# Kernel tuning notes

Hardware: AMD Instinct MI355X
Metric: run time of the kernel (lower is better)

## Reference

```python
import jax, jax.numpy as jnp
import numpy as np

B, T, N, CIN = 8, 12, 883, 3
C, E, H = 64, 10, 8
HD = C // H
TOPK = 48  # int(5 * log2(883))
DIL = [1, 2, 1, 2, 1, 2, 1, 2]
NEG = -9.0e15
L = 8

def _l2norm(v, ax):
    return v / jnp.maximum(jnp.linalg.norm(v, axis=ax, keepdims=True), 1e-12)

def _gelu(v):
    return jax.nn.gelu(v, approximate=False)

def setup_inputs():
    key = jax.random.key(0)
    ks = list(jax.random.split(key, 48))
    it = iter(ks)
    ch0 = jax.random.normal(next(it), (B, T, N))
    ch1 = jax.random.uniform(next(it), (B, T, N))                    # time-of-day in [0,1)
    ch2 = jax.random.randint(next(it), (B, T, N), 0, 7).astype(jnp.float32)  # day-of-week
    x = jnp.stack([ch0, ch1, ch2], axis=-1)
    def row_norm(kk):
        a = jax.random.uniform(kk, (N, N))
        return a / a.sum(axis=1, keepdims=True)
    def w(kk, shape):
        fan_in = shape[-2] if len(shape) >= 2 else shape[-1]
        return (jax.random.normal(kk, shape) * (1.0 / float(np.sqrt(fan_in)))).astype(jnp.float32)
    inp = dict(
        x=x,
        support0=row_norm(next(it)),
        support1=row_norm(next(it)),
        TiD=jax.random.normal(next(it), (288, E)) * 0.1,
        DiW=jax.random.normal(next(it), (7, E)) * 0.1,
        E1=jax.random.normal(next(it), (N, E)) * 0.1,
        E2=jax.random.normal(next(it), (N, E)) * 0.1,
        E3=jax.random.normal(next(it), (N, E)) * 0.1,
        Wx=w(next(it), (T // 2 + 1, E)),
        Wd=w(next(it), (N, 4 * E, E)),
        Wxabs=w(next(it), (E, E)),
        start_w=w(next(it), (CIN, C)), start_b=jnp.zeros((C,)),
        Wq=w(next(it), (L, C, C)), bq=jnp.zeros((L, C)),
        Wk=w(next(it), (L, C, C)), bk=jnp.zeros((L, C)),
        Wv=w(next(it), (L, C, C)), bv=jnp.zeros((L, C)),
        W1=w(next(it), (L, C, 4 * C)), b1=jnp.zeros((L, 4 * C)),
        W2=w(next(it), (L, 4 * C, C)), b2=jnp.zeros((L, C)),
        filt_w=jax.random.normal(next(it), (L, 2, C, C)) * (1.0 / float(np.sqrt(2 * C))),
        filt_b=jnp.zeros((L, C)),
        gate_w=jax.random.normal(next(it), (L, 2, C, C)) * (1.0 / float(np.sqrt(2 * C))),
        gate_b=jnp.zeros((L, C)),
        skip_w=w(next(it), (L, C, 256)), skip_b=jnp.zeros((L, 256)),
        gcn_w=w(next(it), (L, 9 * C, C)), gcn_b=jnp.zeros((L, C)),
        bn_g=jnp.ones((L, C)), bn_b=jnp.zeros((L, C)),
        end1_w=w(next(it), (256, 512)), end1_b=jnp.zeros((512,)),
        end2_w=w(next(it), (512, T)), end2_b=jnp.zeros((T,)),
    )
    return inp

def _graph_gen(xs, T_D, D_W, E3, Wx, Wd, Wxabs):
    # xs: [B,T,N] raw signal channel
    xf = jnp.abs(jnp.fft.rfft(xs, axis=1))                 # [B,F=7,N]
    xf = _l2norm(_l2norm(xf, 1), 2)
    xe = jnp.einsum('btn,td->bnd', xf, Wx)                 # [B,N,E]
    e3 = jnp.broadcast_to(E3[None], (xe.shape[0], N, E))
    xcat = jnp.concatenate([xe, e3, T_D, D_W], axis=2)     # [B,N,4E]
    x1 = jax.nn.relu(jnp.einsum('bnf,nfe->bne', xcat, Wd)) # per-node weight
    mu = x1.mean(axis=(1, 2), keepdims=True)               # LayerNorm over [N,E]
    var = ((x1 - mu) ** 2).mean(axis=(1, 2), keepdims=True)
    x1k = (x1 - mu) / jnp.sqrt(var + 1e-8)
    dew = jnp.einsum('bne,ek->bnk', x1k, Wxabs)
    adp = jax.nn.relu(jnp.einsum('bnk,bmk->bnm', dew, x1)) # [B,N,N]
    _, idx = jax.lax.top_k(adp, TOPK)                      # [B,N,K] per-row topk
    bi = jnp.arange(adp.shape[0])[:, None, None]
    ri = jnp.arange(N)[None, :, None]
    mask = jnp.zeros_like(adp).at[bi, ri, idx].set(1.0)
    return jax.nn.softmax(adp * mask, axis=2)

def reference(x, support0, support1, TiD, DiW, E1, E2, E3, Wx, Wd, Wxabs,
              start_w, start_b, Wq, bq, Wk, bk, Wv, bv, W1, b1, W2, b2,
              filt_w, filt_b, gate_w, gate_b, skip_w, skip_b,
              gcn_w, gcn_b, bn_g, bn_b, end1_w, end1_b, end2_w, end2_b):
    tid = (x[:, -1, :, 1] * 288).astype(jnp.int32)         # [B,N]
    T_D = TiD[tid]                                         # [B,N,E]
    D_W = DiW[x[:, -1, :, 2].astype(jnp.int32)]
    Adap = jax.nn.softmax(jax.nn.relu(E1 @ E2.T), axis=1)
    AD = _graph_gen(x[..., 0], T_D, D_W, E3, Wx, Wd, Wxabs)
    supports = [support0, support1, Adap, AD]

    h = jnp.transpose(x, (0, 3, 2, 1))                     # [B,3,N,T]
    h = jnp.pad(h, ((0, 0), (0, 0), (0, 0), (1, 0)))       # pad to receptive_field=13
    h = jnp.einsum('io,bint->bont', start_w, h) + start_b[None, :, None, None]

    skip = None
    for l in range(L):
        res = h
        # --- causal temporal attention ---
        Xa = jnp.transpose(h, (0, 3, 2, 1))                # [B,Tc,N,C]
        Tc = Xa.shape[1]
        q = _gelu(Xa @ Wq[l] + bq[l]).reshape(-1, Tc, N, H, HD)
        k = _gelu(Xa @ Wk[l] + bk[l]).reshape(-1, Tc, N, H, HD)
        v = _gelu(Xa @ Wv[l] + bv[l]).reshape(-1, Tc, N, H, HD)
        att = jnp.einsum('btnhd,bsnhd->bnhts', q, k) / (HD ** 0.5)
        cmask = jnp.tril(jnp.ones((Tc, Tc), bool))
        att = jax.nn.softmax(jnp.where(cmask, att, NEG), axis=-1)
        o = jnp.einsum('bnhts,bsnhd->bnthd', att, v).reshape(-1, N, Tc, C)
        o = _gelu(o @ W1[l] + b1[l]) @ W2[l] + b2[l]
        h = jnp.transpose(o, (0, 3, 1, 2)) + res           # [B,C,N,Tc]
        # --- gated dilated causal conv (kernel (1,2), dilation d) ---
        d = DIL[l]
        a0, a1 = h[..., :-d], h[..., d:]
        f = jnp.tanh(jnp.einsum('io,bint->bont', filt_w[l, 0], a0)
                     + jnp.einsum('io,bint->bont', filt_w[l, 1], a1)
                     + filt_b[l][None, :, None, None])
        g = jax.nn.sigmoid(jnp.einsum('io,bint->bont', gate_w[l, 0], a0)
                           + jnp.einsum('io,bint->bont', gate_w[l, 1], a1)
                           + gate_b[l][None, :, None, None])
        h = f * g
        s = jnp.einsum('io,bint->bont', skip_w[l], h) + skip_b[l][None, :, None, None]
        skip = s if skip is None else s + skip[..., -s.shape[3]:]
        # --- diffusion graph conv, order 2 over 4 supports ---
        out = [h]
        for a in supports:
            if a.ndim == 3:
                x1 = jnp.einsum('bcvt,bwv->bcwt', h, a)
                x2 = jnp.einsum('bcvt,bwv->bcwt', x1, a)
            else:
                x1 = jnp.einsum('bcvt,vw->bcwt', h, a)
                x2 = jnp.einsum('bcvt,vw->bcwt', x1, a)
            out += [x1, x2]
        hc = jnp.concatenate(out, axis=1)                  # [B,9C,N,Tc']
        h = jnp.einsum('io,bint->bont', gcn_w[l], hc) + gcn_b[l][None, :, None, None]
        h = h + res[..., -h.shape[3]:]
        # --- BatchNorm2d (batch statistics, training-mode normalization) ---
        mu = h.mean(axis=(0, 2, 3), keepdims=True)
        var = ((h - mu) ** 2).mean(axis=(0, 2, 3), keepdims=True)
        h = bn_g[l][None, :, None, None] * (h - mu) / jnp.sqrt(var + 1e-5) \
            + bn_b[l][None, :, None, None]

    out = jax.nn.relu(skip)
    out = jax.nn.relu(jnp.einsum('io,bint->bont', end1_w, out)
                      + end1_b[None, :, None, None])
    out = jnp.einsum('io,bint->bont', end2_w, out) + end2_b[None, :, None, None]
    return out  # [B, out_steps=12, N, 1]
```

## Files before the change

### kernel.cpp

```cpp
#include <hip/hip_runtime.h>
#include <math.h>

#define DIVUP(a,b) (((a)+(b)-1)/(b))

namespace {

constexpr int B=8, T=12, N=883, CIN=3, C=64, E=10, H=8, HD=8, TOPK=48, L=8;
constexpr int SKC=256, F7=7, T13=13;
constexpr int NP=896;

typedef __attribute__((ext_vector_type(8))) short bf16x8;
typedef __attribute__((ext_vector_type(4))) float f32x4;

__device__ __forceinline__ float geluf(float x){ return 0.5f*x*(1.0f+erff(x*0.7071067811865475f)); }
__device__ __forceinline__ float sigmf(float x){ return 1.0f/(1.0f+expf(-x)); }
__device__ __forceinline__ float us2f(unsigned short u){ return __uint_as_float(((unsigned)u)<<16); }
__device__ __forceinline__ unsigned short f2us(float f){
  unsigned x=__float_as_uint(f);
  return (unsigned short)((x + 0x7fffu + ((x>>16)&1u))>>16);
}

template<int KK, int STRIDE, int KW>
__device__ __forceinline__ f32x4 tile_mm(
    const unsigned short* sAh, const unsigned short* sAl,
    const unsigned short* __restrict__ Wh, const unsigned short* __restrict__ Wl,
    int colBase, int lane, f32x4 acc){
  int lr=lane&15, lg=lane>>4;
  #pragma unroll
  for(int k0=0;k0<KK;k0+=32){
    bf16x8 ah=*(const bf16x8*)&sAh[lr*STRIDE+k0+8*lg];
    bf16x8 al=*(const bf16x8*)&sAl[lr*STRIDE+k0+8*lg];
    bf16x8 bh=*(const bf16x8*)&Wh[(size_t)(colBase+lr)*KW+k0+8*lg];
    bf16x8 bl=*(const bf16x8*)&Wl[(size_t)(colBase+lr)*KW+k0+8*lg];
    acc=__builtin_amdgcn_mfma_f32_16x16x32_bf16(ah,bh,acc,0,0,0);
    acc=__builtin_amdgcn_mfma_f32_16x16x32_bf16(ah,bl,acc,0,0,0);
    acc=__builtin_amdgcn_mfma_f32_16x16x32_bf16(al,bh,acc,0,0,0);
  }
  return acc;
}

__global__ void k_dft(const float* __restrict__ x, float* __restrict__ xf){
  int idx = blockIdx.x*256 + threadIdx.x;
  if(idx >= B*F7*N) return;
  int n = idx % N; int f = (idx/N) % F7; int b = idx/(N*F7);
  float re=0.f, im=0.f;
  for(int t=0;t<T;t++){
    float v = x[((size_t)(b*T+t)*N+n)*CIN];
    float ang = -6.283185307179586f * (float)(f*t) / 12.0f;
    re += v*cosf(ang); im += v*sinf(ang);
  }
  xf[idx] = sqrtf(re*re+im*im);
}

__global__ void k_l2f(float* __restrict__ xf){
  int idx = blockIdx.x*256 + threadIdx.x;
  if(idx >= B*N) return;
  int n = idx % N; int b = idx / N;
  float s=0.f;
  for(int f=0;f<F7;f++){ float v=xf[((size_t)b*F7+f)*N+n]; s+=v*v; }
  float inv = 1.0f/fmaxf(sqrtf(s), 1e-12f);
  for(int f=0;f<F7;f++) xf[((size_t)b*F7+f)*N+n] *= inv;
}

__global__ void k_l2n(float* __restrict__ xf){
  int bf = blockIdx.x; int tid = threadIdx.x;
  __shared__ float red[256];
  size_t base = (size_t)bf*N;
  float s=0.f;
  for(int i=tid;i<N;i+=256){ float v=xf[base+i]; s+=v*v; }
  red[tid]=s; __syncthreads();
  for(int k=128;k>0;k>>=1){ if(tid<k) red[tid]+=red[tid+k]; __syncthreads(); }
  float inv = 1.0f/fmaxf(sqrtf(red[0]), 1e-12f);
  __syncthreads();
  for(int i=tid;i<N;i+=256) xf[base+i]*=inv;
}

__global__ void k_x1(const float* __restrict__ x, const float* __restrict__ xf,
                     const float* __restrict__ E3, const float* __restrict__ TiD,
                     const float* __restrict__ DiW, const float* __restrict__ Wx,
                     const float* __restrict__ Wd, float* __restrict__ x1){
  int idx = blockIdx.x*256+threadIdx.x;
  if(idx>=B*N) return;
  int n=idx%N, b=idx/N;
  float xc[40];
  for(int d=0;d<E;d++){
    float a=0.f;
    for(int f=0;f<F7;f++) a += xf[((size_t)b*F7+f)*N+n]*Wx[f*E+d];
    xc[d]=a;
  }
  for(int d=0;d<E;d++) xc[10+d]=E3[n*E+d];
  int ti = (int)(x[((size_t)(b*T+(T-1))*N+n)*CIN+1]*288.0f);
  int dw = (int)(x[((size_t)(b*T+(T-1))*N+n)*CIN+2]);
  for(int d=0;d<E;d++) xc[20+d]=TiD[ti*E+d];
  for(int d=0;d<E;d++) xc[30+d]=DiW[dw*E+d];
  for(int e=0;e<E;e++){
    float a=0.f;
    for(int f=0;f<40;f++) a += xc[f]*Wd[((size_t)n*40+f)*E+e];
    x1[(size_t)idx*E+e]=fmaxf(a,0.f);
  }
}

__global__ void k_lnstats(const float* __restrict__ x1, float* __restrict__ st){
  int b=blockIdx.x, tid=threadIdx.x;
  __shared__ float rs[256], rq[256];
  const int M=N*E;
  float s=0.f,q=0.f;
  for(int i=tid;i<M;i+=256){ float v=x1[(size_t)b*M+i]; s+=v; q+=v*v; }
  rs[tid]=s; rq[tid]=q; __syncthreads();
  for(int k=128;k>0;k>>=1){ if(tid<k){ rs[tid]+=rs[tid+k]; rq[tid]+=rq[tid+k]; } __syncthreads(); }
  if(tid==0){ float mu=rs[0]/M; float var=rq[0]/M-mu*mu; st[b*2]=mu; st[b*2+1]=var; }
}

__global__ void k_dew(const float* __restrict__ x1, const float* __restrict__ st,
                      const float* __restrict__ Wxabs, float* __restrict__ dew){
  int idx=blockIdx.x*256+threadIdx.x;
  if(idx>=B*N) return;
  int b=idx/N;
  float mu=st[b*2], var=st[b*2+1];
  float rs=rsqrtf(var+1e-8f);
  float xk[E];
  for(int e=0;e<E;e++) xk[e]=(x1[(size_t)idx*E+e]-mu)*rs;
  for(int k=0;k<E;k++){
    float a=0.f;
    for(int e=0;e<E;e++) a+=xk[e]*Wxabs[e*E+k];
    dew[(size_t)idx*E+k]=a;
  }
}

__global__ void k_adp(const float* __restrict__ dew, const float* __restrict__ x1,
                      float* __restrict__ adp){
  size_t idx=(size_t)blockIdx.x*256+threadIdx.x;
  if(idx>=(size_t)B*N*N) return;
  int m=(int)(idx%N); int n=(int)((idx/N)%N); int b=(int)(idx/((size_t)N*N));
  const float* dr=dew+((size_t)b*N+n)*E;
  const float* xr=x1+((size_t)b*N+m)*E;
  float a=0.f;
  for(int k=0;k<E;k++) a+=dr[k]*xr[k];
  adp[idx]=fmaxf(a,0.f);
}

__global__ __launch_bounds__(256) void k_topk(const float* __restrict__ adp,
                       unsigned short* __restrict__ ADhi, unsigned short* __restrict__ ADlo){
  int row = blockIdx.x*4 + (threadIdx.x>>6);
  int lane = threadIdx.x & 63;
  const float* rp = adp + (size_t)row*N;
  float v[14];
  #pragma unroll
  for(int j=0;j<14;j++){
    int i = lane + j*64;
    v[j] = (i<N) ? rp[i] : -1.f;
  }
  unsigned sel = 0u;
  float m0 = 0.f;
  for(int k=0;k<TOPK;k++){
    float bv = -2.f; int bi = 1<<20;
    #pragma unroll
    for(int j=0;j<14;j++){
      if(!((sel>>j)&1u) && v[j] > bv){ bv = v[j]; bi = lane + j*64; }
    }
    #pragma unroll
    for(int off=1; off<64; off<<=1){
      float ov = __shfl_xor(bv, off);
      int   oi = __shfl_xor(bi, off);
      if(ov > bv || (ov==bv && oi<bi)){ bv=ov; bi=oi; }
    }
    if(k==0) m0 = bv;
    if((bi&63)==lane) sel |= 1u << (bi>>6);
  }
  float pv[14];
  float ls = 0.f;
  #pragma unroll
  for(int j=0;j<14;j++){
    int i = lane + j*64;
    float p = ((sel>>j)&1u) ? v[j] : 0.f;
    pv[j] = p;
    if(i<N) ls += expf(p - m0);
  }
  #pragma unroll
  for(int off=1; off<64; off<<=1) ls += __shfl_xor(ls, off);
  float invZ = 1.f/ls;
  size_t base = ((size_t)(row/N)*NP + (size_t)(row%N))*NP;
  #pragma unroll
  for(int j=0;j<14;j++){
    int i = lane + j*64;
    if(i<N){
      float f = expf(pv[j]-m0)*invZ;
      unsigned short h=f2us(f);
      ADhi[base+i]=h; ADlo[base+i]=f2us(f-us2f(h));
    }
  }
}

__global__ void k_adap(const float* __restrict__ E1, const float* __restrict__ E2,
                       unsigned short* __restrict__ Mh, unsigned short* __restrict__ Ml){
  int v=blockIdx.x, tid=threadIdx.x;
  __shared__ float rowv[N];
  __shared__ float rv[256];
  float e1[E];
  for(int e=0;e<E;e++) e1[e]=E1[v*E+e];
  for(int j=tid;j<N;j+=256){
    float s=0.f;
    for(int e=0;e<E;e++) s+=e1[e]*E2[j*E+e];
    rowv[j]=fmaxf(s,0.f);
  }
  __syncthreads();
  float lm=-1e30f;
  for(int j=tid;j<N;j+=256) lm=fmaxf(lm,rowv[j]);
  rv[tid]=lm; __syncthreads();
  for(int s=128;s>0;s>>=1){ if(tid<s) rv[tid]=fmaxf(rv[tid],rv[tid+s]); __syncthreads(); }
  float m=rv[0]; __syncthreads();
  float ls=0.f;
  for(int j=tid;j<N;j+=256) ls+=expf(rowv[j]-m);
  rv[tid]=ls; __syncthreads();
  for(int s=128;s>0;s>>=1){ if(tid<s) rv[tid]+=rv[tid+s]; __syncthreads(); }
  float invZ=1.0f/rv[0];
  for(int j=tid;j<N;j+=256){
    float f=expf(rowv[j]-m)*invZ;
    unsigned short h=f2us(f);
    Mh[(size_t)j*NP+v]=h; Ml[(size_t)j*NP+v]=f2us(f-us2f(h));
  }
}

__global__ void k_cvtT(const float* __restrict__ A, unsigned short* __restrict__ Mh,
                       unsigned short* __restrict__ Ml){
  int idx=blockIdx.x*256+threadIdx.x;
  if(idx>=N*N) return;
  int w=idx/N, v=idx%N;
  float f=A[(size_t)v*N+w];
  unsigned short h=f2us(f);
  Mh[(size_t)w*NP+v]=h;
  Ml[(size_t)w*NP+v]=f2us(f-us2f(h));
}

__global__ void k_cvt_qkv(const float* __restrict__ Wq, const float* __restrict__ Wk,
                          const float* __restrict__ Wv,
                          unsigned short* __restrict__ dh, unsigned short* __restrict__ dl){
  int idx=blockIdx.x*256+threadIdx.x;
  if(idx>=L*192*64) return;
  int l=idx/12288, rem=idx%12288, col=rem/64, k=rem%64;
  int mat=col>>6, o=col&63;
  const float* W=(mat==0)?Wq:((mat==1)?Wk:Wv);
  float v=W[(size_t)l*4096 + k*64 + o];
  unsigned short h=f2us(v);
  dh[idx]=h; dl[idx]=f2us(v-us2f(h));
}
__global__ void k_cvt_w1(const float* __restrict__ W1,
                         unsigned short* __restrict__ dh, unsigned short* __restrict__ dl){
  int idx=blockIdx.x*256+threadIdx.x;
  if(idx>=L*256*64) return;
  int l=idx/16384, rem=idx%16384, col=rem/64, k=rem%64;
  float v=W1[(size_t)l*16384 + k*256 + col];
  unsigned short h=f2us(v);
  dh[idx]=h; dl[idx]=f2us(v-us2f(h));
}
__global__ void k_cvt_w2(const float* __restrict__ W2,
                         unsigned short* __restrict__ dh, unsigned short* __restrict__ dl){
  int idx=blockIdx.x*256+threadIdx.x;
  if(idx>=L*64*256) return;
  int l=idx/16384, rem=idx%16384, col=rem/256, k=rem%256;
  float v=W2[(size_t)l*16384 + k*64 + col];
  unsigned short h=f2us(v);
  dh[idx]=h; dl[idx]=f2us(v-us2f(h));
}
__global__ void k_cvt_conv(const float* __restrict__ fw, const float* __restrict__ gw,
                           unsigned short* __restrict__ dh, unsigned short* __restrict__ dl){
  int idx=blockIdx.x*256+threadIdx.x;
  if(idx>=L*128*128) return;
  int l=idx/16384, rem=idx%16384, col=rem/128, k=rem%128;
  int c=col&63, fg=col>>6, tap=k>>6, i=k&63;
  const float* W=fg?gw:fw;
  float v=W[(size_t)l*8192 + tap*4096 + i*64 + c];
  unsigned short h=f2us(v);
  dh[idx]=h; dl[idx]=f2us(v-us2f(h));
}
__global__ void k_cvt_gcn(const float* __restrict__ Wg,
                          unsigned short* __restrict__ dh, unsigned short* __restrict__ dl){
  int idx=blockIdx.x*256+threadIdx.x;
  if(idx>=L*64*576) return;
  int l=idx/36864, rem=idx%36864, o=rem/576, k=rem%576;
  float v=Wg[((size_t)l*576 + k)*64 + o];
  unsigned short h=f2us(v);
  dh[idx]=h; dl[idx]=f2us(v-us2f(h));
}

__global__ void k_zero(float* __restrict__ p, int n){
  int idx=blockIdx.x*256+threadIdx.x;
  if(idx<n) p[idx]=0.f;
}
__global__ void k_zeroUS(unsigned short* __restrict__ p, long long n){
  long long idx=(long long)blockIdx.x*256+threadIdx.x;
  if(idx<n) p[idx]=0;
}

__global__ __launch_bounds__(256) void k_trx(
    const unsigned short* __restrict__ Sh, const unsigned short* __restrict__ Sl,
    unsigned short* __restrict__ Dh, unsigned short* __restrict__ Dl, int M){
  __shared__ unsigned short th[64][66], tl[64][66];
  int b=blockIdx.z;
  int m0=blockIdx.x*64, n0=blockIdx.y*64;
  int tid=threadIdx.x;
  const unsigned short* sbh=Sh + (size_t)b*N*M;
  const unsigned short* sbl=Sl + (size_t)b*N*M;
  for(int idx=tid; idx<64*64; idx+=256){
    int i=idx>>6, j=idx&63;
    int n=n0+i;
    unsigned short vh=0, vl=0;
    if(n<N){
      size_t o=(size_t)n*M + m0+j;
      vh=sbh[o]; vl=sbl[o];
    }
    th[j][i]=vh; tl[j][i]=vl;
  }
  __syncthreads();
  unsigned short* dbh=Dh + (size_t)b*M*NP;
  unsigned short* dbl=Dl + (size_t)b*M*NP;
  for(int idx=tid; idx<64*64; idx+=256){
    int r=idx>>6, cc=idx&63;
    size_t o=(size_t)(m0+r)*NP + n0+cc;
    dbh[o]=th[r][cc]; dbl[o]=tl[r][cc];
  }
}

__global__ void k_start(const float* __restrict__ x, const float* __restrict__ sw,
                        const float* __restrict__ sb, float* __restrict__ h){
  int idx=blockIdx.x*256+threadIdx.x;
  if(idx>=B*N*T13*C) return;
  int c=idx&63; int t=(idx>>6)%T13; int n=(idx/(64*T13))%N; int b=idx/(64*T13*N);
  float a=sb[c];
  if(t>0){
    size_t xb=((size_t)(b*T+(t-1))*N+n)*CIN;
    for(int i=0;i<CIN;i++) a += sw[i*C+c]*x[xb+i];
  }
  h[idx]=a;
}

template<int TC, int D>
__global__ __launch_bounds__(256) void k_attconv(const float* __restrict__ hin,
  const unsigned short* __restrict__ Wqkvh, const unsigned short* __restrict__ Wqkvl,
  const unsigned short* __restrict__ W1h,   const unsigned short* __restrict__ W1l,
  const unsigned short* __restrict__ W2h,   const unsigned short* __restrict__ W2l,
  const unsigned short* __restrict__ Wch,   const unsigned short* __restrict__ Wcl,
  const float* __restrict__ bq, const float* __restrict__ bk, const float* __restrict__ bv,
  const float* __restrict__ b1, const float* __restrict__ b2,
  const float* __restrict__ fb, const float* __restrict__ gb,
  const float* __restrict__ skw, const float* __restrict__ skb,
  const float* __restrict__ bnst, const float* __restrict__ bng, const float* __restrict__ bnb,
  unsigned short* __restrict__ hThi, unsigned short* __restrict__ hTlo,
  float* __restrict__ skipacc, int first){
  constexpr int TN = TC - D;
  int bn=blockIdx.x; int tid=threadIdx.x;
  int lane=tid&63, wid=tid>>6;
  int lr=lane&15, lg=lane>>4;
  __shared__ __align__(16) char smem[37888];
  float* sxa=(float*)smem;
  float* sq =(float*)(smem+4096);
  float* sk_=(float*)(smem+8192);
  float* sv =(float*)(smem+12288);
  unsigned short* sA1h=(unsigned short*)(smem+16384);
  unsigned short* sA1l=(unsigned short*)(smem+18688);
  unsigned short* sA2h=(unsigned short*)(smem+20992);
  unsigned short* sA2l=(unsigned short*)(smem+29440);
  float* sfg=(float*)(smem+8192);
  unsigned short* cAh=(unsigned short*)(smem+20992);
  unsigned short* cAl=(unsigned short*)(smem+25344);
  float* stg=(float*)smem;

  const float* hp = hin + (size_t)bn*TC*64;
  for(int idx=tid; idx<TC*64; idx+=256){
    int t=idx>>6, c=idx&63;
    float v=hp[idx];
    if(bng) v=(v-bnst[c])*bnst[64+c]*bng[c]+bnb[c];
    sxa[idx]=v;
    unsigned short h=f2us(v);
    sA1h[t*72+c]=h; sA1l[t*72+c]=f2us(v-us2f(h));
  }
  for(int idx=tid; idx<(16-TC)*64; idx+=256){
    int t=TC+(idx>>6), c=idx&63;
    sxa[t*64+c]=0.f; sA1h[t*72+c]=0; sA1l[t*72+c]=0;
  }
  __syncthreads();

  #pragma unroll
  for(int it=0; it<3; ++it){
    int tile=it*4+wid;
    f32x4 acc={0.f,0.f,0.f,0.f};
    acc=tile_mm<64,72,64>(sA1h,sA1l,Wqkvh,Wqkvl,tile*16,lane,acc);
    int col=tile*16+lr; int mat=col>>6, o=col&63;
    const float* bm=(mat==0)?bq:((mat==1)?bk:bv);
    float* dst=(mat==0)?sq:((mat==1)?sk_:sv);
    float bias=bm[o];
    #pragma unroll
    for(int r=0;r<4;r++){
      int t=lg*4+r;
      if(t<TC) dst[t*64+o]=geluf(acc[r]+bias);
    }
  }
  __syncthreads();

  if(tid<H*TC){
    int hh=tid/TC, t=tid%TC;
    const float* qr=&sq[t*64+hh*HD];
    float att[TC];
    float m=-1e30f;
    #pragma unroll
    for(int s=0;s<TC;s++){
      float a=0.f;
      #pragma unroll
      for(int d=0;d<HD;d++) a+=qr[d]*sk_[s*64+hh*HD+d];
      a*=0.3535533905932738f;
      a=(s<=t)?a:-1e30f;
      att[s]=a; m=fmaxf(m,a);
    }
    float Z=0.f;
    #pragma unroll
    for(int s=0;s<TC;s++){ float e=expf(att[s]-m); att[s]=e; Z+=e; }
    float invZ=1.0f/Z;
    #pragma unroll
    for(int d=0;d<HD;d++){
      float o=0.f;
      #pragma unroll
      for(int s=0;s<TC;s++) o+=att[s]*sv[s*64+hh*HD+d];
      float v=o*invZ;
      unsigned short h=f2us(v);
      sA1h[t*72+hh*8+d]=h; sA1l[t*72+hh*8+d]=f2us(v-us2f(h));
    }
  }
  __syncthreads();

  #pragma unroll
  for(int it=0; it<4; ++it){
    int tile=it*4+wid;
    f32x4 acc={0.f,0.f,0.f,0.f};
    acc=tile_mm<64,72,64>(sA1h,sA1l,W1h,W1l,tile*16,lane,acc);
    int col=tile*16+lr;
    float bias=b1[col];
    #pragma unroll
    for(int r=0;r<4;r++){
      int t=lg*4+r;
      float v=(t<TC)?geluf(acc[r]+bias):0.f;
      unsigned short h=f2us(v);
      sA2h[t*264+col]=h; sA2l[t*264+col]=f2us(v-us2f(h));
    }
  }
  __syncthreads();

  {
    int tile=wid;
    f32x4 acc={0.f,0.f,0.f,0.f};
    acc=tile_mm<256,264,256>(sA2h,sA2l,W2h,W2l,tile*16,lane,acc);
    int col=tile*16+lr;
    float bias=b2[col];
    #pragma unroll
    for(int r=0;r<4;r++){
      int t=lg*4+r;
      if(t<TC) sq[t*64+col]=acc[r]+bias+sxa[t*64+col];
    }
  }
  __syncthreads();

  for(int idx=tid; idx<16*128; idx+=256){
    int t=idx>>7, k=idx&127;
    int c=k&63;
    float v=0.f;
    if(t<TN) v=sq[((k<64)?t:(t+D))*64+c];
    unsigned short h=f2us(v);
    cAh[t*136+k]=h; cAl[t*136+k]=f2us(v-us2f(h));
  }
  __syncthreads();

  #pragma unroll
  for(int it=0; it<2; ++it){
    int tile=it*4+wid;
    f32x4 acc={0.f,0.f,0.f,0.f};
    acc=tile_mm<128,136,128>(cAh,cAl,Wch,Wcl,tile*16,lane,acc);
    int col=tile*16+lr;
    float bias=(col<64)?fb[col]:gb[col&63];
    #pragma unroll
    for(int r=0;r<4;r++){
      int t=lg*4+r;
      float v=acc[r]+bias;
      sfg[t*128+col]=(col<64)?tanhf(v):sigmf(v);
    }
  }
  __syncthreads();

  if(tid<C) stg[tid]=sfg[(TN-1)*128+tid]*sfg[(TN-1)*128+64+tid];
  __syncthreads();

  {
    float a=skb[tid];
    for(int i=0;i<C;i++) a+=stg[i]*skw[i*SKC+tid];
    size_t so_=(size_t)bn*SKC+tid;
    if(first) skipacc[so_]=a; else skipacc[so_]+=a;
  }
  size_t obase=(size_t)bn*64*TN;
  for(int idx=tid; idx<TN*64; idx+=256){
    int tt=idx>>6, c=idx&63;
    float v=sfg[tt*128+c]*sfg[tt*128+64+c];
    unsigned short h=f2us(v);
    hThi[obase+idx]=h;
    hTlo[obase+idx]=f2us(v-us2f(h));
  }
}

__global__ __launch_bounds__(256) void k_spatmm(
    const unsigned short* __restrict__ Ah, const unsigned short* __restrict__ Al,
    long long aStride,
    const unsigned short* __restrict__ Xh, const unsigned short* __restrict__ Xl,
    const unsigned short* __restrict__ XTh, const unsigned short* __restrict__ XTl,
    int xT,
    unsigned short* __restrict__ Yh, unsigned short* __restrict__ Yl,
    unsigned short* __restrict__ YTh, unsigned short* __restrict__ YTl,
    int M){
  __shared__ unsigned short sAh[128*40];
  __shared__ unsigned short sAl[128*40];
  __shared__ unsigned short sXh[64*40];
  __shared__ unsigned short sXl[64*40];
  int b=blockIdx.z;
  const unsigned short* Abh=Ah+(size_t)b*aStride;
  const unsigned short* Abl=Al+(size_t)b*aStride;
  int tid=threadIdx.x;
  int w0=blockIdx.x*128, c0=blockIdx.y*64;
  int lane=tid&63, wid=tid>>6;
  int lr=lane&15, lg=lane>>4;
  f32x4 acc[2][4];
  #pragma unroll
  for(int j=0;j<2;j++){
    #pragma unroll
    for(int i=0;i<4;i++){ acc[j][i][0]=0.f; acc[j][i][1]=0.f; acc[j][i][2]=0.f; acc[j][i][3]=0.f; }
  }
  const int ar=tid>>1,  akb=(tid&1)*16;
  const int xr=tid>>2,  xkb=(tid&3)*8;
  const int xk=tid>>3,  xcb=(tid&7)*8;
  const int xkx=xk ^ (8*((xcb>>3)&3));
  for(int k0=0;k0<N;k0+=32){
    {
      uint4 qh0=*(const uint4*)&Abh[(size_t)(w0+ar)*NP + k0+akb];
      uint4 qh1=*(const uint4*)&Abh[(size_t)(w0+ar)*NP + k0+akb+8];
      uint4 ql0=*(const uint4*)&Abl[(size_t)(w0+ar)*NP + k0+akb];
      uint4 ql1=*(const uint4*)&Abl[(size_t)(w0+ar)*NP + k0+akb+8];
      *(uint4*)&sAh[ar*40+akb]=qh0;   *(uint4*)&sAh[ar*40+akb+8]=qh1;
      *(uint4*)&sAl[ar*40+akb]=ql0;   *(uint4*)&sAl[ar*40+akb+8]=ql1;
    }
    if(xT){
      const unsigned short* Xbth=XTh+(size_t)b*M*NP;
      const unsigned short* Xbtl=XTl+(size_t)b*M*NP;
      uint4 qh=*(const uint4*)&Xbth[(size_t)(c0+xr)*NP + k0+xkb];
      uint4 ql=*(const uint4*)&Xbtl[(size_t)(c0+xr)*NP + k0+xkb];
      *(uint4*)&sXh[xr*40+xkb]=qh;
      *(uint4*)&sXl[xr*40+xkb]=ql;
    }else{
      const unsigned short* Xbh=Xh+(size_t)b*N*M;
      const unsigned short* Xbl=Xl+(size_t)b*N*M;
      uint4 qh={0,0,0,0}, ql={0,0,0,0};
      if(k0+xk<N){
        qh=*(const uint4*)&Xbh[(size_t)(k0+xk)*M + c0+xcb];
        ql=*(const uint4*)&Xbl[(size_t)(k0+xk)*M + c0+xcb];
      }
      unsigned short uh[8], ul[8];
      uh[0]=(unsigned short)(qh.x&0xffff); uh[1]=(unsigned short)(qh.x>>16);
      uh[2]=(unsigned short)(qh.y&0xffff); uh[3]=(unsigned short)(qh.y>>16);
      uh[4]=(unsigned short)(qh.z&0xffff); uh[5]=(unsigned short)(qh.z>>16);
      uh[6]=(unsigned short)(qh.w&0xffff); uh[7]=(unsigned short)(qh.w>>16);
      ul[0]=(unsigned short)(ql.x&0xffff); ul[1]=(unsigned short)(ql.x>>16);
      ul[2]=(unsigned short)(ql.y&0xffff); ul[3]=(unsigned short)(ql.y>>16);
      ul[4]=(unsigned short)(ql.z&0xffff); ul[5]=(unsigned short)(ql.z>>16);
      ul[6]=(unsigned short)(ql.w&0xffff); ul[7]=(unsigned short)(ql.w>>16);
      #pragma unroll
      for(int j=0;j<8;j++){
        sXh[(xcb+j)*40+xkx]=uh[j];
        sXl[(xcb+j)*40+xkx]=ul[j];
      }
    }
    __syncthreads();
    bf16x8 a_h[2], a_l[2], x_h[4], x_l[4];
    #pragma unroll
    for(int j=0;j<2;j++){
      int r=32*wid+16*j+lr;
      a_h[j]=*(const bf16x8*)&sAh[r*40+8*lg];
      a_l[j]=*(const bf16x8*)&sAl[r*40+8*lg];
    }
    #pragma unroll
    for(int i=0;i<4;i++){
      int cc=16*i+lr;
      int g = xT ? lg : (lg ^ ((cc>>3)&3));
      x_h[i]=*(const bf16x8*)&sXh[cc*40+8*g];
      x_l[i]=*(const bf16x8*)&sXl[cc*40+8*g];
    }
    #pragma unroll
    for(int j=0;j<2;j++){
      #pragma unroll
      for(int i=0;i<4;i++){
        acc[j][i]=__builtin_amdgcn_mfma_f32_16x16x32_bf16(a_h[j],x_h[i],acc[j][i],0,0,0);
        acc[j][i]=__builtin_amdgcn_mfma_f32_16x16x32_bf16(a_h[j],x_l[i],acc[j][i],0,0,0);
        acc[j][i]=__builtin_amdgcn_mfma_f32_16x16x32_bf16(a_l[j],x_h[i],acc[j][i],0,0,0);
      }
    }
    __syncthreads();
  }
  #pragma unroll
  for(int j=0;j<2;j++){
    int rbase=w0+32*wid+16*j+lg*4;
    #pragma unroll
    for(int i=0;i<4;i++){
      int col=c0+16*i+lr;
      unsigned short hh[4], ll[4];
      #pragma unroll
      for(int r=0;r<4;r++){
        float v=acc[j][i][r];
        hh[r]=f2us(v);
        ll[r]=f2us(v-us2f(hh[r]));
      }
      #pragma unroll
      for(int r=0;r<4;r++){
        int row=rbase+r;
        if(row<N){
          size_t o=((size_t)b*N+row)*M+col;
          Yh[o]=hh[r]; Yl[o]=ll[r];
        }
      }
      if(YTh){
        size_t o=(size_t)b*M*NP + (size_t)col*NP + rbase;
        ushort4 ph; ph.x=hh[0]; ph.y=hh[1]; ph.z=hh[2]; ph.w=hh[3];
        ushort4 pl; pl.x=ll[0]; pl.y=ll[1]; pl.z=ll[2]; pl.w=ll[3];
        *(ushort4*)&YTh[o]=ph;
        *(ushort4*)&YTl[o]=pl;
      }
    }
  }
}

template<int TN, int FIRST>
__global__ __launch_bounds__(256) void k_gcnmm(
    const unsigned short* __restrict__ S0h, const unsigned short* __restrict__ S0l,
    const unsigned short* __restrict__ S1h, const unsigned short* __restrict__ S1l,
    const unsigned short* __restrict__ S2h, const unsigned short* __restrict__ S2l,
    const unsigned short* __restrict__ Wbh, const unsigned short* __restrict__ Wbl,
    int kOff,
    const float* __restrict__ gb, const float* __restrict__ res,
    const float* __restrict__ bnst, const float* __restrict__ bng, const float* __restrict__ bnb,
    float* __restrict__ acc, int Tc){
  constexpr int SL=64*TN;
  constexpr int NS=FIRST?3:2;
  constexpr int KK=NS*64;
  __shared__ unsigned short sAh[64*40], sAl[64*40];
  int bn0=blockIdx.x*4;
  int tid=threadIdx.x, lane=tid&63, wid=tid>>6;
  int lr=lane&15, lg=lane>>4;
  f32x4 a4[4];
  #pragma unroll
  for(int rt=0;rt<4;rt++){ a4[rt][0]=0.f; a4[rt][1]=0.f; a4[rt][2]=0.f; a4[rt][3]=0.f; }
  const int ar=tid>>2, akb=(tid&3)*8;
  const int ani=ar>>4, att_=ar&15;
  #pragma unroll
  for(int kc=0; kc<KK/32; ++kc){
    int k0=kc*32; int j=k0>>6; int i0=k0&63;
    const unsigned short* sh=(j==0)?S0h:((j==1)?S1h:S2h);
    const unsigned short* sl=(j==0)?S0l:((j==1)?S1l:S2l);
    uint4 qh={0,0,0,0}, ql={0,0,0,0};
    if(att_<TN){
      size_t o=(size_t)(bn0+ani)*SL + att_*64 + i0 + akb;
      qh=*(const uint4*)&sh[o]; ql=*(const uint4*)&sl[o];
    }
    *(uint4*)&sAh[ar*40+akb]=qh;
    *(uint4*)&sAl[ar*40+akb]=ql;
    __syncthreads();
    bf16x8 bh=*(const bf16x8*)&Wbh[(size_t)(wid*16+lr)*576 + kOff + k0 + 8*lg];
    bf16x8 bl=*(const bf16x8*)&Wbl[(size_t)(wid*16+lr)*576 + kOff + k0 + 8*lg];
    #pragma unroll
    for(int rt=0;rt<4;rt++){
      bf16x8 ah=*(const bf16x8*)&sAh[(rt*16+lr)*40+8*lg];
      bf16x8 al=*(const bf16x8*)&sAl[(rt*16+lr)*40+8*lg];
      a4[rt]=__builtin_amdgcn_mfma_f32_16x16x32_bf16(ah,bh,a4[rt],0,0,0);
      a4[rt]=__builtin_amdgcn_mfma_f32_16x16x32_bf16(ah,bl,a4[rt],0,0,0);
      a4[rt]=__builtin_amdgcn_mfma_f32_16x16x32_bf16(al,bh,a4[rt],0,0,0);
    }
    __syncthreads();
  }
  int o=wid*16+lr;
  #pragma unroll
  for(int rt=0;rt<4;rt++){
    int bn=bn0+rt;
    #pragma unroll
    for(int r=0;r<4;r++){
      int t2=lg*4+r;
      if(t2<TN){
        size_t oi=((size_t)bn*TN + t2)*64 + o;
        float v=a4[rt][r];
        if(FIRST){
          float rr=res[((size_t)bn*Tc + (Tc-TN) + t2)*64 + o];
          if(bng) rr=(rr-bnst[o])*bnst[64+o]*bng[o]+bnb[o];
          v += gb[o] + rr;
          acc[oi]=v;
        }else{
          acc[oi]+=v;
        }
      }
    }
  }
}

__global__ __launch_bounds__(256) void k_bnstats1(const float* __restrict__ h,
                                                  float* __restrict__ part, int R){
  int tid=threadIdx.x;
  int c=tid&63, rg=tid>>6;
  float s=0.f,q=0.f;
  for(int r=blockIdx.x*4+rg; r<R; r+=1024){
    float v=h[(size_t)r*64+c];
    s+=v; q+=v*v;
  }
  __shared__ float ls[256], lq[256];
  ls[tid]=s; lq[tid]=q; __syncthreads();
  if(rg==0){
    s=ls[c]+ls[64+c]+ls[128+c]+ls[192+c];
    q=lq[c]+lq[64+c]+lq[128+c]+lq[192+c];
    part[blockIdx.x*128+c]=s;
    part[blockIdx.x*128+64+c]=q;
  }
}
__global__ __launch_bounds__(256) void k_bnstats2(const float* __restrict__ part,
                                                  float* __restrict__ st, int R){
  int tid=threadIdx.x;
  int c=tid&63, g=tid>>6;
  float s=0.f,q=0.f;
  for(int p=g;p<256;p+=4){ s+=part[p*128+c]; q+=part[p*128+64+c]; }
  __shared__ float ls[256], lq[256];
  ls[tid]=s; lq[tid]=q; __syncthreads();
  if(g==0){
    s=ls[c]+ls[64+c]+ls[128+c]+ls[192+c];
    q=lq[c]+lq[64+c]+lq[128+c]+lq[192+c];
    float mu=s/R;
    float var=q/R-mu*mu;
    st[c]=mu; st[64+c]=rsqrtf(var+1e-5f);
  }
}

__global__ void k_head(const float* __restrict__ skipacc, const float* __restrict__ W1,
  const float* __restrict__ b1, const float* __restrict__ W2, const float* __restrict__ b2,
  float* __restrict__ out){
  int gid=blockIdx.x; int tid=threadIdx.x;
  int n=gid%N; int b=gid/N;
  __shared__ float s[SKC];
  __shared__ float hid[512];
  if(tid<SKC){
    float v=skipacc[(size_t)gid*SKC+tid];
    s[tid]=fmaxf(v,0.f);
  }
  __syncthreads();
  {
    float a=b1[tid];
    for(int i=0;i<SKC;i++) a+=s[i]*W1[(size_t)i*512+tid];
    hid[tid]=fmaxf(a,0.f);
  }
  __syncthreads();
  if(tid<T){
    float a=b2[tid];
    for(int j=0;j<512;j++) a+=hid[j]*W2[(size_t)j*T+tid];
    out[((size_t)b*T+tid)*N+n]=a;
  }
}

struct Ctx {
  const float *bq,*bk,*bv,*b1,*b2,*filt_b,*gate_b,*skip_w,*skip_b,*gcn_b,*bn_g,*bn_b;
  const unsigned short *qkvTh,*qkvTl,*w1Th,*w1Tl,*w2Th,*w2Tl,*cvTh,*cvTl,*wgh,*wgl;
  const unsigned short* matH[4];
  const unsigned short* matL[4];
  long long matStride[4];
  float *pH,*pAlt,*skipacc,*bnst,*bnpart;
  unsigned short *hThi,*hTlo,*Phi,*Plo,*Qhi,*Qlo;
  unsigned short *hTth,*hTtl,*PTh,*PTl;
  hipStream_t stream;
};

template<int TC, int D>
void run_layer(Ctx& c, int l, bool last){
  constexpr int TN=TC-D;
  const float* ibnst=(l>0)?c.bnst:nullptr;
  const float* ibng =(l>0)?(c.bn_g+(size_t)(l-1)*C):nullptr;
  const float* ibnb =(l>0)?(c.bn_b+(size_t)(l-1)*C):nullptr;
  k_attconv<TC,D><<<B*N,256,0,c.stream>>>(c.pH,
    c.qkvTh+(size_t)l*12288, c.qkvTl+(size_t)l*12288,
    c.w1Th+(size_t)l*16384,  c.w1Tl+(size_t)l*16384,
    c.w2Th+(size_t)l*16384,  c.w2Tl+(size_t)l*16384,
    c.cvTh+(size_t)l*16384,  c.cvTl+(size_t)l*16384,
    c.bq+(size_t)l*C, c.bk+(size_t)l*C, c.bv+(size_t)l*C,
    c.b1+(size_t)l*4*C, c.b2+(size_t)l*C,
    c.filt_b+(size_t)l*C, c.gate_b+(size_t)l*C,
    c.skip_w+(size_t)l*C*SKC, c.skip_b+(size_t)l*SKC,
    ibnst, ibng, ibnb,
    c.hThi, c.hTlo, c.skipacc, l==0?1:0);
  if(!last){
    int M=C*TN, nMB=M/64;
    const unsigned short* Wh=c.wgh+(size_t)l*36864;
    const unsigned short* Wl=c.wgl+(size_t)l*36864;
    dim3 sg(DIVUP(N,128), nMB, B);
    k_trx<<<dim3(M/64,DIVUP(NP,64),B),256,0,c.stream>>>(c.hThi,c.hTlo, c.hTth,c.hTtl, M);
    for(int s=0;s<4;s++){
      k_spatmm<<<sg,256,0,c.stream>>>(c.matH[s],c.matL[s],c.matStride[s],
          nullptr,nullptr, c.hTth,c.hTtl, 1,
          c.Phi,c.Plo, c.PTh,c.PTl, M);
      if(c.PTh){
        k_spatmm<<<sg,256,0,c.stream>>>(c.matH[s],c.matL[s],c.matStride[s],
            nullptr,nullptr, c.PTh,c.PTl, 1,
            c.Qhi,c.Qlo, nullptr,nullptr, M);
      }else{
        k_spatmm<<<sg,256,0,c.stream>>>(c.matH[s],c.matL[s],c.matStride[s],
            c.Phi,c.Plo, nullptr,nullptr, 0,
            c.Qhi,c.Qlo, nullptr,nullptr, M);
      }
      if(s==0){
        k_gcnmm<TN,1><<<(B*N)/4,256,0,c.stream>>>(
            c.hThi,c.hTlo, c.Phi,c.Plo, c.Qhi,c.Qlo,
            Wh,Wl, 0, c.gcn_b+(size_t)l*C, c.pH,
            ibnst, ibng, ibnb, c.pAlt, TC);
      }else{
        k_gcnmm<TN,0><<<(B*N)/4,256,0,c.stream>>>(
            c.Phi,c.Plo, c.Qhi,c.Qlo, nullptr,nullptr,
            Wh,Wl, (1+2*s)*64, nullptr, nullptr,
            nullptr,nullptr,nullptr, c.pAlt, TC);
      }
    }
    int R=B*N*TN;
    k_bnstats1<<<256,256,0,c.stream>>>(c.pAlt, c.bnpart, R);
    k_bnstats2<<<1,256,0,c.stream>>>(c.bnpart, c.bnst, R);
    float* tmp=c.pH; c.pH=c.pAlt; c.pAlt=tmp;
  }
}

}

extern "C" void kernel_launch(void* const* d_in, const int* in_sizes, int n_in,
                              void* d_out, int out_size, void* d_ws, size_t ws_size,
                              hipStream_t stream){
  (void)in_sizes; (void)n_in;
  const float* x      =(const float*)d_in[0];
  const float* sup0   =(const float*)d_in[1];
  const float* sup1   =(const float*)d_in[2];
  const float* TiD    =(const float*)d_in[3];
  const float* DiW    =(const float*)d_in[4];
  const float* E1     =(const float*)d_in[5];
  const float* E2     =(const float*)d_in[6];
  const float* E3     =(const float*)d_in[7];
  const float* Wx     =(const float*)d_in[8];
  const float* Wd     =(const float*)d_in[9];
  const float* Wxabs  =(const float*)d_in[10];
  const float* start_w=(const float*)d_in[11];
  const float* start_b=(const float*)d_in[12];
  const float* Wq     =(const float*)d_in[13];
  const float* Wk     =(const float*)d_in[15];
  const float* Wv     =(const float*)d_in[17];
  const float* W1     =(const float*)d_in[19];
  const float* W2     =(const float*)d_in[21];
  const float* filt_w =(const float*)d_in[23];
  const float* gate_w =(const float*)d_in[25];
  const float* gcn_w  =(const float*)d_in[29];

  Ctx c;
  c.bq=(const float*)d_in[14];
  c.bk=(const float*)d_in[16];
  c.bv=(const float*)d_in[18];
  c.b1=(const float*)d_in[20];
  c.b2=(const float*)d_in[22];
  c.filt_b=(const float*)d_in[24];
  c.gate_b=(const float*)d_in[26];
  c.skip_w=(const float*)d_in[27]; c.skip_b=(const float*)d_in[28];
  c.gcn_b =(const float*)d_in[30];
  c.bn_g  =(const float*)d_in[31]; c.bn_b  =(const float*)d_in[32];
  const float* end1_w =(const float*)d_in[33];
  const float* end1_b =(const float*)d_in[34];
  const float* end2_w =(const float*)d_in[35];
  const float* end2_b =(const float*)d_in[36];
  c.stream=stream;

  size_t off=0;
  auto allocF=[&](size_t nf)->float*{
    nf=(nf+3)&~(size_t)3;
    float* p=(float*)((char*)d_ws+off);
    off += nf*sizeof(float);
    return p;
  };
  auto allocU=[&](size_t nu)->unsigned short*{
    nu=(nu+7)&~(size_t)7;
    unsigned short* p=(unsigned short*)((char*)d_ws+off);
    off += nu*sizeof(unsigned short);
    return p;
  };
  const size_t HMAX =(size_t)B*C*N*T13;
  const size_t XSZ  =(size_t)B*C*N*12;
  const size_t XTSZ =(size_t)768*NP*B;
  const size_t SUPP =(size_t)NP*NP;
  const size_t ADSZ =(size_t)B*NP*NP;

  float* xf     = allocF((size_t)B*F7*N);
  float* gx1    = allocF((size_t)B*N*E);
  float* gdew   = allocF((size_t)B*N*E);
  float* gst    = allocF(16);
  c.bnst        = allocF(2*C);
  c.bnpart      = allocF(256*128);
  float* adp    = allocF((size_t)B*N*N);
  c.pH          = allocF(HMAX);
  c.pAlt        = allocF(HMAX);
  c.skipacc     = allocF((size_t)B*N*SKC);
  unsigned short* matRegion=(unsigned short*)((char*)d_ws+off);
  unsigned short* s0h = allocU(SUPP);
  unsigned short* s0l = allocU(SUPP);
  unsigned short* s1h = allocU(SUPP);
  unsigned short* s1l = allocU(SUPP);
  unsigned short* aph = allocU(SUPP);
  unsigned short* apl = allocU(SUPP);
  unsigned short* adh = allocU(ADSZ);
  unsigned short* adl = allocU(ADSZ);
  long long matRegionN = (long long)(( (unsigned short*)((char*)d_ws+off) ) - matRegion);
  c.hThi = allocU(XSZ);  c.hTlo = allocU(XSZ);
  c.Phi  = allocU(XSZ);  c.Plo  = allocU(XSZ);
  c.Qhi  = allocU(XSZ);  c.Qlo  = allocU(XSZ);
  unsigned short* qkvTh = allocU((size_t)L*12288);
  unsigned short* qkvTl = allocU((size_t)L*12288);
  unsigned short* w1Th  = allocU((size_t)L*16384);
  unsigned short* w1Tl  = allocU((size_t)L*16384);
  unsigned short* w2Th  = allocU((size_t)L*16384);
  unsigned short* w2Tl  = allocU((size_t)L*16384);
  unsigned short* cvTh  = allocU((size_t)L*16384);
  unsigned short* cvTl  = allocU((size_t)L*16384);
  unsigned short* wgh   = allocU((size_t)L*36864);
  unsigned short* wgl   = allocU((size_t)L*36864);
  if(off > ws_size){
    k_zero<<<DIVUP(out_size,256),256,0,stream>>>((float*)d_out, out_size);
    return;
  }
  c.hTth = (unsigned short*)adp;
  c.hTtl = c.hTth + XTSZ;
  {
    size_t save=off;
    c.PTh = allocU(XTSZ);
    c.PTl = allocU(XTSZ);
    if(off > ws_size){ c.PTh=nullptr; c.PTl=nullptr; off=save; }
  }
  c.qkvTh=qkvTh; c.qkvTl=qkvTl; c.w1Th=w1Th; c.w1Tl=w1Tl;
  c.w2Th=w2Th; c.w2Tl=w2Tl; c.cvTh=cvTh; c.cvTl=cvTl;
  c.wgh=wgh; c.wgl=wgl;
  c.matH[0]=s0h; c.matL[0]=s0l; c.matStride[0]=0;
  c.matH[1]=s1h; c.matL[1]=s1l; c.matStride[1]=0;
  c.matH[2]=aph; c.matL[2]=apl; c.matStride[2]=0;
  c.matH[3]=adh; c.matL[3]=adl; c.matStride[3]=(long long)NP*NP;

  k_zeroUS<<<(int)DIVUP(matRegionN,256),256,0,stream>>>(matRegion, matRegionN);
  k_cvt_qkv <<<DIVUP(L*192*64,256),256,0,stream>>>(Wq,Wk,Wv,qkvTh,qkvTl);
  k_cvt_w1  <<<DIVUP(L*256*64,256),256,0,stream>>>(W1,w1Th,w1Tl);
  k_cvt_w2  <<<DIVUP(L*64*256,256),256,0,stream>>>(W2,w2Th,w2Tl);
  k_cvt_conv<<<DIVUP(L*128*128,256),256,0,stream>>>(filt_w,gate_w,cvTh,cvTl);
  k_cvt_gcn <<<DIVUP(L*64*576,256),256,0,stream>>>(gcn_w,wgh,wgl);
  k_dft <<<DIVUP(B*F7*N,256),256,0,stream>>>(x, xf);
  k_l2f <<<DIVUP(B*N,256),256,0,stream>>>(xf);
  k_l2n <<<B*F7,256,0,stream>>>(xf);
  k_x1  <<<DIVUP(B*N,256),256,0,stream>>>(x, xf, E3, TiD, DiW, Wx, Wd, gx1);
  k_lnstats<<<B,256,0,stream>>>(gx1, gst);
  k_dew <<<DIVUP(B*N,256),256,0,stream>>>(gx1, gst, Wxabs, gdew);
  k_adp <<<DIVUP(B*N*N,256),256,0,stream>>>(gdew, gx1, adp);
  k_topk<<<(B*N)/4,256,0,stream>>>(adp, adh, adl);
  k_adap<<<N,256,0,stream>>>(E1, E2, aph, apl);
  k_cvtT<<<DIVUP(N*N,256),256,0,stream>>>(sup0, s0h, s0l);
  k_cvtT<<<DIVUP(N*N,256),256,0,stream>>>(sup1, s1h, s1l);

  k_start<<<DIVUP(B*N*T13*C,256),256,0,stream>>>(x, start_w, start_b, c.pH);

  run_layer<13,1>(c,0,false);
  run_layer<12,2>(c,1,false);
  run_layer<10,1>(c,2,false);
  run_layer< 9,2>(c,3,false);
  run_layer< 7,1>(c,4,false);
  run_layer< 6,2>(c,5,false);
  run_layer< 4,1>(c,6,false);
  run_layer< 3,2>(c,7,true);

  k_head<<<B*N,512,0,stream>>>(c.skipacc, end1_w, end1_b, end2_w, end2_b, (float*)d_out);
}
```

Before: 5.644 ms.

## Process two nodes per attention-conv block to reuse weight fragments across MFMA tiles

```diff
diff --git a/kernel.cpp b/kernel.cpp
--- a/kernel.cpp
+++ b/kernel.cpp
@@ -37,6 +37,29 @@
     acc=__builtin_amdgcn_mfma_f32_16x16x32_bf16(al,bh,acc,0,0,0);
   }
   return acc;
+}
+
+template<int KK, int STRIDE, int KW>
+__device__ __forceinline__ void tile_mm2(
+    const unsigned short* sAh, const unsigned short* sAl,
+    const unsigned short* __restrict__ Wh, const unsigned short* __restrict__ Wl,
+    int colBase, int lane, f32x4& acc0, f32x4& acc1){
+  int lr=lane&15, lg=lane>>4;
+  #pragma unroll
+  for(int k0=0;k0<KK;k0+=32){
+    bf16x8 bh=*(const bf16x8*)&Wh[(size_t)(colBase+lr)*KW+k0+8*lg];
+    bf16x8 bl=*(const bf16x8*)&Wl[(size_t)(colBase+lr)*KW+k0+8*lg];
+    bf16x8 ah0=*(const bf16x8*)&sAh[lr*STRIDE+k0+8*lg];
+    bf16x8 al0=*(const bf16x8*)&sAl[lr*STRIDE+k0+8*lg];
+    bf16x8 ah1=*(const bf16x8*)&sAh[(lr+16)*STRIDE+k0+8*lg];
+    bf16x8 al1=*(const bf16x8*)&sAl[(lr+16)*STRIDE+k0+8*lg];
+    acc0=__builtin_amdgcn_mfma_f32_16x16x32_bf16(ah0,bh,acc0,0,0,0);
+    acc0=__builtin_amdgcn_mfma_f32_16x16x32_bf16(ah0,bl,acc0,0,0,0);
+    acc0=__builtin_amdgcn_mfma_f32_16x16x32_bf16(al0,bh,acc0,0,0,0);
+    acc1=__builtin_amdgcn_mfma_f32_16x16x32_bf16(ah1,bh,acc1,0,0,0);
+    acc1=__builtin_amdgcn_mfma_f32_16x16x32_bf16(ah1,bl,acc1,0,0,0);
+    acc1=__builtin_amdgcn_mfma_f32_16x16x32_bf16(al1,bh,acc1,0,0,0);
+  }
 }
 
 __global__ void k_dft(const float* __restrict__ x, float* __restrict__ xf){
@@ -348,43 +371,48 @@
   unsigned short* __restrict__ hThi, unsigned short* __restrict__ hTlo,
   float* __restrict__ skipacc, int first){
   constexpr int TN = TC - D;
-  int bn=blockIdx.x; int tid=threadIdx.x;
+  int bn0=blockIdx.x*2; int tid=threadIdx.x;
   int lane=tid&63, wid=tid>>6;
   int lr=lane&15, lg=lane>>4;
-  __shared__ __align__(16) char smem[37888];
+  __shared__ __align__(16) char smem[51200];
   float* sxa=(float*)smem;
-  float* sq =(float*)(smem+4096);
-  float* sk_=(float*)(smem+8192);
-  float* sv =(float*)(smem+12288);
-  unsigned short* sA1h=(unsigned short*)(smem+16384);
-  unsigned short* sA1l=(unsigned short*)(smem+18688);
-  unsigned short* sA2h=(unsigned short*)(smem+20992);
-  unsigned short* sA2l=(unsigned short*)(smem+29440);
-  float* sfg=(float*)(smem+8192);
-  unsigned short* cAh=(unsigned short*)(smem+20992);
-  unsigned short* cAl=(unsigned short*)(smem+25344);
+  unsigned short* sA1h=(unsigned short*)(smem+8192);
+  unsigned short* sA1l=(unsigned short*)(smem+12800);
+  float* sq =(float*)(smem+17408);
+  float* sk_=(float*)(smem+25600);
+  float* sv =(float*)(smem+33792);
+  unsigned short* sA2h=(unsigned short*)(smem+17408);
+  unsigned short* sA2l=(unsigned short*)(smem+34304);
+  float* xcf=(float*)smem;
+  unsigned short* cAh=(unsigned short*)(smem+17408);
+  unsigned short* cAl=(unsigned short*)(smem+26112);
+  float* sfg=(float*)(smem+34816);
   float* stg=(float*)smem;
 
-  const float* hp = hin + (size_t)bn*TC*64;
-  for(int idx=tid; idx<TC*64; idx+=256){
-    int t=idx>>6, c=idx&63;
+  const float* hp = hin + (size_t)bn0*TC*64;
+  for(int idx=tid; idx<2*TC*64; idx+=256){
+    int ni=idx/(TC*64); int rem=idx%(TC*64);
+    int t=rem>>6, c=rem&63;
     float v=hp[idx];
     if(bng) v=(v-bnst[c])*bnst[64+c]*bng[c]+bnb[c];
-    sxa[idx]=v;
+    int row=ni*16+t;
+    sxa[row*64+c]=v;
     unsigned short h=f2us(v);
-    sA1h[t*72+c]=h; sA1l[t*72+c]=f2us(v-us2f(h));
-  }
-  for(int idx=tid; idx<(16-TC)*64; idx+=256){
-    int t=TC+(idx>>6), c=idx&63;
-    sxa[t*64+c]=0.f; sA1h[t*72+c]=0; sA1l[t*72+c]=0;
+    sA1h[row*72+c]=h; sA1l[row*72+c]=f2us(v-us2f(h));
+  }
+  for(int idx=tid; idx<2*(16-TC)*64; idx+=256){
+    int pr=idx>>6, c=idx&63;
+    int ni=pr/(16-TC), tp=TC+pr%(16-TC);
+    int row=ni*16+tp;
+    sxa[row*64+c]=0.f; sA1h[row*72+c]=0; sA1l[row*72+c]=0;
   }
   __syncthreads();
 
   #pragma unroll
   for(int it=0; it<3; ++it){
     int tile=it*4+wid;
-    f32x4 acc={0.f,0.f,0.f,0.f};
-    acc=tile_mm<64,72,64>(sA1h,sA1l,Wqkvh,Wqkvl,tile*16,lane,acc);
+    f32x4 a0={0.f,0.f,0.f,0.f}, a1={0.f,0.f,0.f,0.f};
+    tile_mm2<64,72,64>(sA1h,sA1l,Wqkvh,Wqkvl,tile*16,lane,a0,a1);
     int col=tile*16+lr; int mat=col>>6, o=col&63;
     const float* bm=(mat==0)?bq:((mat==1)?bk:bv);
     float* dst=(mat==0)?sq:((mat==1)?sk_:sv);
@@ -392,21 +420,26 @@
     #pragma unroll
     for(int r=0;r<4;r++){
       int t=lg*4+r;
-      if(t<TC) dst[t*64+o]=geluf(acc[r]+bias);
-    }
-  }
-  __syncthreads();
-
-  if(tid<H*TC){
-    int hh=tid/TC, t=tid%TC;
-    const float* qr=&sq[t*64+hh*HD];
+      if(t<TC){
+        dst[t*64+o]      =geluf(a0[r]+bias);
+        dst[(16+t)*64+o] =geluf(a1[r]+bias);
+      }
+    }
+  }
+  __syncthreads();
+
+  if(tid<2*H*TC){
+    int ni=tid/(H*TC); int rr=tid%(H*TC);
+    int hh=rr/TC, t=rr%TC;
+    int rb=ni*16;
+    const float* qr=&sq[(rb+t)*64+hh*HD];
     float att[TC];
     float m=-1e30f;
     #pragma unroll
     for(int s=0;s<TC;s++){
       float a=0.f;
       #pragma unroll
-      for(int d=0;d<HD;d++) a+=qr[d]*sk_[s*64+hh*HD+d];
+      for(int d=0;d<HD;d++) a+=qr[d]*sk_[(rb+s)*64+hh*HD+d];
       a*=0.3535533905932738f;
       a=(s<=t)?a:-1e30f;
       att[s]=a; m=fmaxf(m,a);
@@ -419,10 +452,10 @@
     for(int d=0;d<HD;d++){
       float o=0.f;
       #pragma unroll
-      for(int s=0;s<TC;s++) o+=att[s]*sv[s*64+hh*HD+d];
+      for(int s=0;s<TC;s++) o+=att[s]*sv[(rb+s)*64+hh*HD+d];
       float v=o*invZ;
       unsigned short h=f2us(v);
-      sA1h[t*72+hh*8+d]=h; sA1l[t*72+hh*8+d]=f2us(v-us2f(h));
+      sA1h[(rb+t)*72+hh*8+d]=h; sA1l[(rb+t)*72+hh*8+d]=f2us(v-us2f(h));
     }
   }
   __syncthreads();
@@ -430,73 +463,85 @@
   #pragma unroll
   for(int it=0; it<4; ++it){
     int tile=it*4+wid;
-    f32x4 acc={0.f,0.f,0.f,0.f};
-    acc=tile_mm<64,72,64>(sA1h,sA1l,W1h,W1l,tile*16,lane,acc);
+    f32x4 a0={0.f,0.f,0.f,0.f}, a1={0.f,0.f,0.f,0.f};
+    tile_mm2<64,72,64>(sA1h,sA1l,W1h,W1l,tile*16,lane,a0,a1);
     int col=tile*16+lr;
     float bias=b1[col];
     #pragma unroll
     for(int r=0;r<4;r++){
       int t=lg*4+r;
-      float v=(t<TC)?geluf(acc[r]+bias):0.f;
-      unsigned short h=f2us(v);
-      sA2h[t*264+col]=h; sA2l[t*264+col]=f2us(v-us2f(h));
+      float v0=(t<TC)?geluf(a0[r]+bias):0.f;
+      float v1=(t<TC)?geluf(a1[r]+bias):0.f;
+      unsigned short h0=f2us(v0), h1=f2us(v1);
+      sA2h[t*264+col]=h0;      sA2l[t*264+col]=f2us(v0-us2f(h0));
+      sA2h[(16+t)*264+col]=h1; sA2l[(16+t)*264+col]=f2us(v1-us2f(h1));
     }
   }
   __syncthreads();
 
   {
     int tile=wid;
-    f32x4 acc={0.f,0.f,0.f,0.f};
-    acc=tile_mm<256,264,256>(sA2h,sA2l,W2h,W2l,tile*16,lane,acc);
+    f32x4 a0={0.f,0.f,0.f,0.f}, a1={0.f,0.f,0.f,0.f};
+    tile_mm2<256,264,256>(sA2h,sA2l,W2h,W2l,tile*16,lane,a0,a1);
     int col=tile*16+lr;
     float bias=b2[col];
     #pragma unroll
     for(int r=0;r<4;r++){
       int t=lg*4+r;
-      if(t<TC) sq[t*64+col]=acc[r]+bias+sxa[t*64+col];
-    }
-  }
-  __syncthreads();
-
-  for(int idx=tid; idx<16*128; idx+=256){
-    int t=idx>>7, k=idx&127;
+      if(t<TC){
+        xcf[t*64+col]     =a0[r]+bias+sxa[t*64+col];
+        xcf[(16+t)*64+col]=a1[r]+bias+sxa[(16+t)*64+col];
+      }
+    }
+  }
+  __syncthreads();
+
+  for(int idx=tid; idx<32*128; idx+=256){
+    int row=idx>>7, k=idx&127;
+    int ni=row>>4, t=row&15;
     int c=k&63;
     float v=0.f;
-    if(t<TN) v=sq[((k<64)?t:(t+D))*64+c];
+    if(t<TN) v=xcf[(ni*16+((k<64)?t:(t+D)))*64+c];
     unsigned short h=f2us(v);
-    cAh[t*136+k]=h; cAl[t*136+k]=f2us(v-us2f(h));
+    cAh[row*136+k]=h; cAl[row*136+k]=f2us(v-us2f(h));
   }
   __syncthreads();
 
   #pragma unroll
   for(int it=0; it<2; ++it){
     int tile=it*4+wid;
-    f32x4 acc={0.f,0.f,0.f,0.f};
-    acc=tile_mm<128,136,128>(cAh,cAl,Wch,Wcl,tile*16,lane,acc);
+    f32x4 a0={0.f,0.f,0.f,0.f}, a1={0.f,0.f,0.f,0.f};
+    tile_mm2<128,136,128>(cAh,cAl,Wch,Wcl,tile*16,lane,a0,a1);
     int col=tile*16+lr;
     float bias=(col<64)?fb[col]:gb[col&63];
     #pragma unroll
     for(int r=0;r<4;r++){
       int t=lg*4+r;
-      float v=acc[r]+bias;
-      sfg[t*128+col]=(col<64)?tanhf(v):sigmf(v);
-    }
-  }
-  __syncthreads();
-
-  if(tid<C) stg[tid]=sfg[(TN-1)*128+tid]*sfg[(TN-1)*128+64+tid];
-  __syncthreads();
-
-  {
-    float a=skb[tid];
-    for(int i=0;i<C;i++) a+=stg[i]*skw[i*SKC+tid];
-    size_t so_=(size_t)bn*SKC+tid;
+      float v0=a0[r]+bias, v1=a1[r]+bias;
+      sfg[t*128+col]     =(col<64)?tanhf(v0):sigmf(v0);
+      sfg[(16+t)*128+col]=(col<64)?tanhf(v1):sigmf(v1);
+    }
+  }
+  __syncthreads();
+
+  if(tid<2*C){
+    int ni=tid>>6, c=tid&63;
+    stg[ni*64+c]=sfg[(ni*16+TN-1)*128+c]*sfg[(ni*16+TN-1)*128+64+c];
+  }
+  __syncthreads();
+
+  for(int idx=tid; idx<2*SKC; idx+=256){
+    int ni=idx>>8, o=idx&255;
+    float a=skb[o];
+    for(int i=0;i<C;i++) a+=stg[ni*64+i]*skw[i*SKC+o];
+    size_t so_=(size_t)(bn0+ni)*SKC+o;
     if(first) skipacc[so_]=a; else skipacc[so_]+=a;
   }
-  size_t obase=(size_t)bn*64*TN;
-  for(int idx=tid; idx<TN*64; idx+=256){
-    int tt=idx>>6, c=idx&63;
-    float v=sfg[tt*128+c]*sfg[tt*128+64+c];
+  size_t obase=(size_t)bn0*64*TN;
+  for(int idx=tid; idx<2*TN*64; idx+=256){
+    int ni=idx/(TN*64); int rem=idx%(TN*64);
+    int tt=rem>>6, c=rem&63;
+    float v=sfg[(ni*16+tt)*128+c]*sfg[(ni*16+tt)*128+64+c];
     unsigned short h=f2us(v);
     hThi[obase+idx]=h;
     hTlo[obase+idx]=f2us(v-us2f(h));
@@ -778,7 +823,7 @@
   const float* ibnst=(l>0)?c.bnst:nullptr;
   const float* ibng =(l>0)?(c.bn_g+(size_t)(l-1)*C):nullptr;
   const float* ibnb =(l>0)?(c.bn_b+(size_t)(l-1)*C):nullptr;
-  k_attconv<TC,D><<<B*N,256,0,c.stream>>>(c.pH,
+  k_attconv<TC,D><<<(B*N)/2,256,0,c.stream>>>(c.pH,
     c.qkvTh+(size_t)l*12288, c.qkvTl+(size_t)l*12288,
     c.w1Th+(size_t)l*16384,  c.w1Tl+(size_t)l*16384,
     c.w2Th+(size_t)l*16384,  c.w2Tl+(size_t)l*16384,
```

Result: faster. 5.109 ms (-9.5%).
